# Kernel optimization log

Measured on AMD Instinct MI355X. Metric: run time of the kernel, lower is better.

The kernel has to match this reference:

```python
import jax, jax.numpy as jnp
import numpy as np

N, E, D = 100000, 200000, 300
NUM_EDGE_EMB = [6, 3]
BN_EPS = 1e-5


def setup_inputs() -> dict:
    key = jax.random.key(0)
    ks = jax.random.split(key, 10)
    return {
        "node_feats": jax.random.normal(ks[0], (N, D), jnp.float32),
        "src": jax.random.randint(ks[1], (E,), 0, N),
        "dst": jax.random.randint(ks[2], (E,), 0, N),
        "edge_feat0": jax.random.randint(ks[3], (E,), 0, NUM_EDGE_EMB[0]),
        "edge_feat1": jax.random.randint(ks[4], (E,), 0, NUM_EDGE_EMB[1]),
        # edge 'MLP' with num_layers=1 == Linear(num_emb, D) on one-hot indices
        "emb_w0": jax.random.normal(ks[5], (NUM_EDGE_EMB[0], D), jnp.float32) * 0.1,
        "emb_b0": jnp.zeros((D,), jnp.float32),
        "emb_w1": jax.random.normal(ks[6], (NUM_EDGE_EMB[1], D), jnp.float32) * 0.1,
        "emb_b1": jnp.zeros((D,), jnp.float32),
        # GIN update MLP: Linear(D, 2D) -> ReLU -> Linear(2D, D)
        "mlp_w1": jax.random.normal(ks[7], (D, 2 * D), jnp.float32) * (1.0 / np.sqrt(D)),
        "mlp_b1": jnp.zeros((2 * D,), jnp.float32),
        "mlp_w2": jax.random.normal(ks[8], (2 * D, D), jnp.float32) * (1.0 / np.sqrt(2 * D)),
        "mlp_b2": jnp.zeros((D,), jnp.float32),
        "bn_gamma": jnp.ones((D,), jnp.float32),
        "bn_beta": jnp.zeros((D,), jnp.float32),
    }


def reference(node_feats, src, dst, edge_feat0, edge_feat1,
              emb_w0, emb_b0, emb_w1, emb_b1,
              mlp_w1, mlp_b1, mlp_w2, mlp_b2,
              bn_gamma, bn_beta):
    n = node_feats.shape[0]
    # sum of per-variable edge embeddings (one-hot linear == lookup + bias)
    edge_emb = (emb_w0[edge_feat0] + emb_b0) + (emb_w1[edge_feat1] + emb_b1)  # (E, D)
    # u_add_e message, sum-reduce onto destination nodes
    msgs = node_feats[src] + edge_emb                                         # (E, D)
    agg = jax.ops.segment_sum(msgs, dst, num_segments=n)                      # (N, D)
    # GIN update MLP
    h = jax.nn.relu(agg @ mlp_w1 + mlp_b1)
    h = h @ mlp_w2 + mlp_b2
    # BatchNorm1d (training-mode forward: biased batch stats)
    mean = jnp.mean(h, axis=0)
    var = jnp.var(h, axis=0)
    h = (h - mean) * jax.lax.rsqrt(var + BN_EPS) * bn_gamma + bn_beta
    return h
```

## Files before the change

### kernel.cpp

```cpp
#include <hip/hip_runtime.h>
#include <stdint.h>


typedef __attribute__((ext_vector_type(8))) short short8;
typedef __attribute__((ext_vector_type(4))) short short4v;
typedef __attribute__((ext_vector_type(4))) float float4v;

__device__ inline float b2f(unsigned short u) {
  union { unsigned int i; float f; } v; v.i = ((unsigned int)u) << 16; return v.f;
}
__device__ inline unsigned short f2b(float f) {
  union { float f; unsigned int i; } v; v.f = f;
  unsigned int i = v.i;
  i += 0x7fffu + ((i >> 16) & 1u);
  return (unsigned short)(i >> 16);
}

__device__ __forceinline__ void gl_lds16(const short* g, short* l) {
  __builtin_amdgcn_global_load_lds(
      (const __attribute__((address_space(1))) unsigned int*)g,
      (__attribute__((address_space(3))) unsigned int*)l,
      16, 0, 0);
}

__global__ void transpose_pad(const float* __restrict__ in, short* __restrict__ out,
                              int R, int C, int outStride, int total) {
  int idx = blockIdx.x * blockDim.x + threadIdx.x;
  if (idx >= total) return;
  int r = idx / C, c = idx - r * C;
  out[(size_t)c * outStride + r] = (short)f2b(in[idx]);
}

__global__ void nf2b(const float* __restrict__ nf, unsigned short* __restrict__ nfb,
                     int D, int ldab, int total) {
  int idx = blockIdx.x * blockDim.x + threadIdx.x;
  if (idx >= total) return;
  const int chunks = ldab >> 3;
  int node = idx / chunks, c = idx - node * chunks;
  int d = c * 8;
  short4v r0 = {0, 0, 0, 0}, r1 = {0, 0, 0, 0};
  const float* p = &nf[(size_t)node * D + d];
  if (d + 3 < D) {
    float4v v = *(const float4v*)p;
    r0[0] = (short)f2b(v[0]); r0[1] = (short)f2b(v[1]);
    r0[2] = (short)f2b(v[2]); r0[3] = (short)f2b(v[3]);
  }
  if (d + 7 < D) {
    float4v v = *(const float4v*)(p + 4);
    r1[0] = (short)f2b(v[0]); r1[1] = (short)f2b(v[1]);
    r1[2] = (short)f2b(v[2]); r1[3] = (short)f2b(v[3]);
  }
  unsigned short* op = &nfb[(size_t)node * ldab + d];
  *(short4v*)op = r0;
  *(short4v*)(op + 4) = r1;
}

__global__ void build_w01b(const float* __restrict__ w0, const float* __restrict__ w1,
                           const float* __restrict__ b0, const float* __restrict__ b1,
                           unsigned short* __restrict__ w01b, float* __restrict__ bb01,
                           int D, int NUM1, int ldab, int total) {
  int i = blockIdx.x * blockDim.x + threadIdx.x;
  if (i >= total) return;
  int f01 = i / ldab, d = i - f01 * ldab;
  int f0 = f01 / NUM1, f1 = f01 - f0 * NUM1;
  float v = (d < D) ? (w0[f0 * D + d] + w1[f1 * D + d]) : 0.f;
  w01b[i] = f2b(v);
  if (f01 == 0) bb01[d] = (d < D) ? (b0[d] + b1[d]) : 0.f;
}

__global__ void count_deg(const int* __restrict__ dst, int* __restrict__ deg, int E) {
  int e = blockIdx.x * blockDim.x + threadIdx.x;
  if (e < E) atomicAdd(&deg[dst[e]], 1);
}

__global__ void scan1(const int* __restrict__ deg, int* __restrict__ offp,
                      int* __restrict__ bsum, int n) {
  __shared__ int sh[256];
  const int t = threadIdx.x;
  const int base = blockIdx.x * 1024 + t * 4;
  int v[4], s = 0;
#pragma unroll
  for (int j = 0; j < 4; ++j) { int i = base + j; v[j] = (i < n) ? deg[i] : 0; s += v[j]; }
  sh[t] = s;
  __syncthreads();
  for (int d = 1; d < 256; d <<= 1) {
    int x = (t >= d) ? sh[t - d] : 0;
    __syncthreads();
    sh[t] += x;
    __syncthreads();
  }
  int excl = (t > 0) ? sh[t - 1] : 0;
  if (t == 255) bsum[blockIdx.x] = sh[255];
#pragma unroll
  for (int j = 0; j < 4; ++j) { int i = base + j; if (i < n) offp[i] = excl; excl += v[j]; }
}

__global__ void scan2(int* __restrict__ bsum, int nb) {
  __shared__ int sh[256];
  const int t = threadIdx.x;
  sh[t] = (t < nb) ? bsum[t] : 0;
  __syncthreads();
  for (int d = 1; d < 256; d <<= 1) {
    int x = (t >= d) ? sh[t - d] : 0;
    __syncthreads();
    sh[t] += x;
    __syncthreads();
  }
  if (t < nb) bsum[t] = (t > 0) ? sh[t - 1] : 0;
}

__global__ void fill_csr(const int* __restrict__ dst, const int* __restrict__ src,
                         const int* __restrict__ ef0, const int* __restrict__ ef1,
                         const int* __restrict__ offp, const int* __restrict__ bsum,
                         int* __restrict__ tmp, int2* __restrict__ ebp, int NUM1, int E) {
  int e = blockIdx.x * blockDim.x + threadIdx.x;
  if (e >= E) return;
  int dn = dst[e];
  int pos = offp[dn] + bsum[dn >> 10] + atomicAdd(&tmp[dn], 1);
  ebp[pos] = make_int2(src[e], ef0[e] * NUM1 + ef1[e]);
}

__global__ void gather_agg(const unsigned short* __restrict__ nfb,
                           const unsigned short* __restrict__ w01b,
                           const float* __restrict__ bb01,
                           const int* __restrict__ deg, const int* __restrict__ offp,
                           const int* __restrict__ bsum, const int2* __restrict__ ebp,
                           unsigned short* __restrict__ aggb,
                           int ldab, int total) {
  int idx = blockIdx.x * blockDim.x + threadIdx.x;
  if (idx >= total) return;
  const int segs = ldab >> 5;
  int node = idx / segs;
  int c = idx - node * segs;
  int d = c * 32;
  int dg = deg[node];
  int o = offp[node] + bsum[node >> 10];
  float acc[32];
#pragma unroll
  for (int k = 0; k < 32; ++k) acc[k] = 0.f;
  for (int j = 0; j < dg; ++j) {
    int2 p = ebp[o + j];
    const unsigned short* np = &nfb[(size_t)p.x * ldab + d];
    const unsigned short* wp = &w01b[(size_t)p.y * ldab + d];
#pragma unroll
    for (int q = 0; q < 4; ++q) {
      short8 nv = *(const short8*)(np + q * 8);
      short8 wv = *(const short8*)(wp + q * 8);
#pragma unroll
      for (int k = 0; k < 8; ++k)
        acc[q * 8 + k] += b2f((unsigned short)nv[k]) + b2f((unsigned short)wv[k]);
    }
  }
  float fdg = (float)dg;
#pragma unroll
  for (int q = 0; q < 8; ++q) {
    float4v bb = *(const float4v*)&bb01[d + q * 4];
#pragma unroll
    for (int k = 0; k < 4; ++k) acc[q * 4 + k] += fdg * bb[k];
  }
#pragma unroll
  for (int q = 0; q < 4; ++q) {
    short8 r;
#pragma unroll
    for (int k = 0; k < 8; ++k) r[k] = (short)f2b(acc[q * 8 + k]);
    *(short8*)&aggb[(size_t)node * ldab + d + q * 8] = r;
  }
}

template<bool RELU, bool STATS, bool CF32>
__global__ __launch_bounds__(256, 6)
void gemm_lds(const short* __restrict__ A, int lda,
              const short* __restrict__ BT, int ldbt,
              const float* __restrict__ bias,
              void* __restrict__ Cv, int ldc, int storeN,
              int M, int Nn, int KP, int ncolb,
              float* __restrict__ colsum, float* __restrict__ colsumsq) {
  constexpr int BM = 128, BN = 64, BK = 32;
  __shared__ __align__(16) short Al[2][BM * BK];
  __shared__ __align__(16) short Bl[2][BN * BK];

  const int nwg = gridDim.x;
  const int b = blockIdx.x;
  const int qq = nwg >> 3, rr = nwg & 7;
  const int xcd = b & 7, ii = b >> 3;
  const int w = ((xcd < rr) ? xcd * (qq + 1) : rr * (qq + 1) + (xcd - rr) * qq) + ii;
  const int by = w / ncolb, bx = w - by * ncolb;
  const int m0 = by * BM, n0 = bx * BN;

  const int t = threadIdx.x;
  const int wave = t >> 6, lane = t & 63, quad = lane >> 4, lr = lane & 15;
  const int wm = (wave >> 1) * 64, wn = (wave & 1) * 32;

  const int au = lane & 3;
  const int arow0 = (wave * 2 + 0) * 16 + (lane >> 2);
  const int arow1 = (wave * 2 + 1) * 16 + (lane >> 2);
  const int asw0 = au ^ ((arow0 ^ (arow0 >> 2)) & 3);
  const int asw1 = au ^ ((arow1 ^ (arow1 >> 2)) & 3);
  const short* asrc0 = A + (size_t)(m0 + arow0) * lda + asw0 * 8;
  const short* asrc1 = A + (size_t)(m0 + arow1) * lda + asw1 * 8;
  const int adst0 = (wave * 2 + 0) * 512;
  const int adst1 = (wave * 2 + 1) * 512;
  const int brow = wave * 16 + (lane >> 2);
  const int bsw = au ^ ((brow ^ (brow >> 2)) & 3);
  const short* bsrc = BT + (size_t)(n0 + brow) * ldbt + bsw * 8;
  const int bdst = wave * 512;

  int aoff[4], boff[2];
#pragma unroll
  for (int mi = 0; mi < 4; ++mi) {
    int r = wm + mi * 16 + lr;
    aoff[mi] = r * BK + (quad ^ ((r ^ (r >> 2)) & 3)) * 8;
  }
#pragma unroll
  for (int ni = 0; ni < 2; ++ni) {
    int r = wn + ni * 16 + lr;
    boff[ni] = r * BK + (quad ^ ((r ^ (r >> 2)) & 3)) * 8;
  }

  const float4v fzero = {0.f, 0.f, 0.f, 0.f};
  float4v acc[4][2];
#pragma unroll
  for (int mi = 0; mi < 4; ++mi) {
    acc[mi][0] = fzero; acc[mi][1] = fzero;
  }

  const int KPfull = KP & ~63;
  for (int k0 = 0; k0 < KPfull; k0 += 2 * BK) {
    __syncthreads();
    gl_lds16(asrc0 + k0, (short*)&Al[0][adst0]);
    gl_lds16(asrc1 + k0, (short*)&Al[0][adst1]);
    gl_lds16(bsrc + k0, (short*)&Bl[0][bdst]);
    gl_lds16(asrc0 + k0 + BK, (short*)&Al[1][adst0]);
    gl_lds16(asrc1 + k0 + BK, (short*)&Al[1][adst1]);
    gl_lds16(bsrc + k0 + BK, (short*)&Bl[1][bdst]);
    __syncthreads();
#pragma unroll
    for (int p = 0; p < 2; ++p) {
      short8 af[4], bfr[2];
#pragma unroll
      for (int mi = 0; mi < 4; ++mi) af[mi] = *(const short8*)&Al[p][aoff[mi]];
#pragma unroll
      for (int ni = 0; ni < 2; ++ni) bfr[ni] = *(const short8*)&Bl[p][boff[ni]];
#pragma unroll
      for (int mi = 0; mi < 4; ++mi) {
        acc[mi][0] = __builtin_amdgcn_mfma_f32_16x16x32_bf16(af[mi], bfr[0], acc[mi][0], 0, 0, 0);
        acc[mi][1] = __builtin_amdgcn_mfma_f32_16x16x32_bf16(af[mi], bfr[1], acc[mi][1], 0, 0, 0);
      }
    }
  }
  if (KP & 63) {
    int k0 = KPfull;
    __syncthreads();
    gl_lds16(asrc0 + k0, (short*)&Al[0][adst0]);
    gl_lds16(asrc1 + k0, (short*)&Al[0][adst1]);
    gl_lds16(bsrc + k0, (short*)&Bl[0][bdst]);
    __syncthreads();
    short8 af[4], bfr[2];
#pragma unroll
    for (int mi = 0; mi < 4; ++mi) af[mi] = *(const short8*)&Al[0][aoff[mi]];
#pragma unroll
    for (int ni = 0; ni < 2; ++ni) bfr[ni] = *(const short8*)&Bl[0][boff[ni]];
#pragma unroll
    for (int mi = 0; mi < 4; ++mi) {
      acc[mi][0] = __builtin_amdgcn_mfma_f32_16x16x32_bf16(af[mi], bfr[0], acc[mi][0], 0, 0, 0);
      acc[mi][1] = __builtin_amdgcn_mfma_f32_16x16x32_bf16(af[mi], bfr[1], acc[mi][1], 0, 0, 0);
    }
  }

#pragma unroll
  for (int ni = 0; ni < 2; ++ni) {
    int gn = n0 + wn + ni * 16 + lr;
    bool store_c = (gn < storeN);
    bool ncol = (gn < Nn);
    float bv = ncol ? bias[gn] : 0.f;
    float s = 0.f, q = 0.f;
#pragma unroll
    for (int mi = 0; mi < 4; ++mi) {
      int gmb = m0 + wm + mi * 16 + quad * 4;
#pragma unroll
      for (int r = 0; r < 4; ++r) {
        int gm = gmb + r;
        float v = acc[mi][ni][r] + bv;
        if (RELU) v = fmaxf(v, 0.f);
        if (gm < M && store_c) {
          if constexpr (CF32) ((float*)Cv)[(size_t)gm * ldc + gn] = v;
          else ((unsigned short*)Cv)[(size_t)gm * ldc + gn] = f2b(v);
          if (STATS && ncol) { s += v; q += v * v; }
        }
      }
    }
    if constexpr (STATS) {
      s += __shfl_xor(s, 16); q += __shfl_xor(q, 16);
      s += __shfl_xor(s, 32); q += __shfl_xor(q, 32);
      if (quad == 0 && ncol) {
        unsafeAtomicAdd(&colsum[gn], s);
        unsafeAtomicAdd(&colsumsq[gn], q);
      }
    }
  }
}

__global__ void bn_finalize(const float* __restrict__ colsum, const float* __restrict__ colsumsq,
                            const float* __restrict__ gamma, const float* __restrict__ beta,
                            float2* __restrict__ ss, int D, float invN) {
  int d = blockIdx.x * blockDim.x + threadIdx.x;
  if (d >= D) return;
  float mean = colsum[d] * invN;
  float var = fmaxf(colsumsq[d] * invN - mean * mean, 0.f);
  float sc = rsqrtf(var + 1e-5f) * gamma[d];
  float sh = beta[d] - mean * sc;
  ss[d] = make_float2(sc, sh);
}

__global__ void bn_apply4(float4v* __restrict__ out, const float2* __restrict__ ss,
                          int total4, int cquads) {
  int idx = blockIdx.x * blockDim.x + threadIdx.x;
  if (idx >= total4) return;
  int c = (idx % cquads) * 4;
  float4v v = out[idx];
  float2 p0 = ss[c], p1 = ss[c + 1], p2 = ss[c + 2], p3 = ss[c + 3];
  v[0] = v[0] * p0.x + p0.y;
  v[1] = v[1] * p1.x + p1.y;
  v[2] = v[2] * p2.x + p2.y;
  v[3] = v[3] * p3.x + p3.y;
  out[idx] = v;
}

__global__ void bn_apply1(float* __restrict__ out, const float2* __restrict__ ss,
                          int total, int D) {
  int idx = blockIdx.x * blockDim.x + threadIdx.x;
  if (idx >= total) return;
  float2 p = ss[idx % D];
  out[idx] = out[idx] * p.x + p.y;
}

extern "C" void kernel_launch(void* const* d_in, const int* in_sizes, int n_in,
                              void* d_out, int out_size, void* d_ws, size_t ws_size,
                              hipStream_t stream) {
  const float* nf  = (const float*)d_in[0];
  const int*   src = (const int*)d_in[1];
  const int*   dst = (const int*)d_in[2];
  const int*   ef0 = (const int*)d_in[3];
  const int*   ef1 = (const int*)d_in[4];
  const float* ew0 = (const float*)d_in[5];
  const float* eb0 = (const float*)d_in[6];
  const float* ew1 = (const float*)d_in[7];
  const float* eb1 = (const float*)d_in[8];
  const float* w1  = (const float*)d_in[9];
  const float* b1  = (const float*)d_in[10];
  const float* w2  = (const float*)d_in[11];
  const float* b2  = (const float*)d_in[12];
  const float* gam = (const float*)d_in[13];
  const float* bet = (const float*)d_in[14];

  const int D = in_sizes[13];
  const int N = in_sizes[0] / D;
  const int E = in_sizes[1];
  const int H = in_sizes[10];
  const int NUM0 = in_sizes[5] / D;
  const int NUM1 = in_sizes[7] / D;
  const int KP1 = (D + 63) / 64 * 64;
  const int KP2 = (H + 31) / 32 * 32;
  const int NCB1 = (H + 63) / 64;
  const int NCB2 = (D + 63) / 64;
  const int BROWS1 = NCB1 * 64;
  const int BROWS2 = NCB2 * 64;
  const int nrowb = (N + 127) / 128;
  const int MP = nrowb * 128;
  const int nb  = (N + 1023) / 1024;

  char* ws = (char*)d_ws;
  size_t off = 0;
  float* colsum   = (float*)(ws + off); off += 4096;
  float* colsumsq = (float*)(ws + off); off += 4096;
  short* wT1      = (short*)(ws + off); off += (size_t)BROWS1 * KP1 * 2;
  short* wT2      = (short*)(ws + off); off += (size_t)BROWS2 * KP2 * 2;
  int*   deg      = (int*)(ws + off);   off += (size_t)N * 4;
  int*   tmp      = (int*)(ws + off);   off += (size_t)N * 4;
  size_t zero_bytes = off;
  float2* ss      = (float2*)(ws + off); off += 4096;
  unsigned short* w01b = (unsigned short*)(ws + off); off += (size_t)NUM0 * NUM1 * KP1 * 2;
  float* bb01     = (float*)(ws + off);  off += (size_t)KP1 * 4;
  int*   offp     = (int*)(ws + off);    off += (size_t)N * 4;
  int*   bsum     = (int*)(ws + off);    off += 4096;
  int2*  ebp      = (int2*)(ws + off);   off += (size_t)E * 8;
  unsigned short* aggb = (unsigned short*)(ws + off); off += (size_t)MP * KP1 * 2;
  short* h1       = (short*)(ws + off);  off += (size_t)MP * KP2 * 2;
  unsigned short* nfb = (unsigned short*)h1;

  hipMemsetAsync(d_ws, 0, zero_bytes, stream);

  {
    int tot = D * H;
    transpose_pad<<<(tot + 255) / 256, 256, 0, stream>>>(w1, wT1, D, H, KP1, tot);
  }
  {
    int tot = H * D;
    transpose_pad<<<(tot + 255) / 256, 256, 0, stream>>>(w2, wT2, H, D, KP2, tot);
  }
  {
    int tot = NUM0 * NUM1 * KP1;
    build_w01b<<<(tot + 255) / 256, 256, 0, stream>>>(ew0, ew1, eb0, eb1,
                                                      w01b, bb01, D, NUM1, KP1, tot);
  }
  {
    int tot = N * (KP1 / 8);
    nf2b<<<(tot + 255) / 256, 256, 0, stream>>>(nf, nfb, D, KP1, tot);
  }
  count_deg<<<(E + 255) / 256, 256, 0, stream>>>(dst, deg, E);
  scan1<<<nb, 256, 0, stream>>>(deg, offp, bsum, N);
  scan2<<<1, 256, 0, stream>>>(bsum, nb);
  fill_csr<<<(E + 255) / 256, 256, 0, stream>>>(dst, src, ef0, ef1, offp, bsum, tmp,
                                                ebp, NUM1, E);
  {
    int total = N * (KP1 / 32);
    gather_agg<<<(total + 255) / 256, 256, 0, stream>>>(
        nfb, w01b, bb01, deg, offp, bsum, ebp, aggb, KP1, total);
  }
  {
    gemm_lds<true, false, false><<<nrowb * NCB1, 256, 0, stream>>>(
        (const short*)aggb, KP1, wT1, KP1, b1,
        h1, KP2, KP2, N, H, KP1, NCB1, nullptr, nullptr);
  }
  {
    gemm_lds<false, true, true><<<nrowb * NCB2, 256, 0, stream>>>(
        h1, KP2, wT2, KP2, b2,
        d_out, D, D, N, D, KP2, NCB2, colsum, colsumsq);
  }
  bn_finalize<<<(D + 255) / 256, 256, 0, stream>>>(colsum, colsumsq, gam, bet, ss, D,
                                                   1.0f / (float)N);
  if ((D & 3) == 0) {
    int total4 = N * (D / 4);
    bn_apply4<<<(total4 + 255) / 256, 256, 0, stream>>>((float4v*)d_out, ss, total4, D / 4);
  } else {
    int tot = N * D;
    bn_apply1<<<(tot + 255) / 256, 256, 0, stream>>>((float*)d_out, ss, tot, D);
  }
}
```

Before: 559.8 us.

## Replace direct global-to-LDS loads with register-staged loads into padded LDS

The bf16 MFMA GEMM now copies A and B tiles through registers into a padded shared-memory layout (row stride 40), instead of using async global_load_lds with XOR swizzling. It uses a single buffer and one 32-wide K step per iteration, which doubles the number of barriers per K. The occupancy hint in the launch bounds is dropped, and K padding for the first GEMM is rounded to 32 instead of 64. The aim is simpler, conflict-free LDS access. The cost is extra register traffic and barriers, and less overlap between loads and MFMA work.

```diff
diff --git a/kernel.cpp b/kernel.cpp
--- a/kernel.cpp
+++ b/kernel.cpp
@@ -14,13 +14,6 @@
   unsigned int i = v.i;
   i += 0x7fffu + ((i >> 16) & 1u);
   return (unsigned short)(i >> 16);
-}
-
-__device__ __forceinline__ void gl_lds16(const short* g, short* l) {
-  __builtin_amdgcn_global_load_lds(
-      (const __attribute__((address_space(1))) unsigned int*)g,
-      (__attribute__((address_space(3))) unsigned int*)l,
-      16, 0, 0);
 }
 
 __global__ void transpose_pad(const float* __restrict__ in, short* __restrict__ out,
@@ -168,16 +161,16 @@
 }
 
 template<bool RELU, bool STATS, bool CF32>
-__global__ __launch_bounds__(256, 6)
-void gemm_lds(const short* __restrict__ A, int lda,
-              const short* __restrict__ BT, int ldbt,
-              const float* __restrict__ bias,
-              void* __restrict__ Cv, int ldc, int storeN,
-              int M, int Nn, int KP, int ncolb,
-              float* __restrict__ colsum, float* __restrict__ colsumsq) {
-  constexpr int BM = 128, BN = 64, BK = 32;
-  __shared__ __align__(16) short Al[2][BM * BK];
-  __shared__ __align__(16) short Bl[2][BN * BK];
+__global__ __launch_bounds__(256)
+void gemm_rs(const short* __restrict__ A, int lda,
+             const short* __restrict__ BT, int ldbt,
+             const float* __restrict__ bias,
+             void* __restrict__ Cv, int ldc, int storeN,
+             int M, int Nn, int KP, int ncolb,
+             float* __restrict__ colsum, float* __restrict__ colsumsq) {
+  constexpr int BM = 128, BN = 64, BK = 32, SA = 40;
+  __shared__ __align__(16) short Al[BM * SA];
+  __shared__ __align__(16) short Bl[BN * SA];
 
   const int nwg = gridDim.x;
   const int b = blockIdx.x;
@@ -191,32 +184,6 @@
   const int wave = t >> 6, lane = t & 63, quad = lane >> 4, lr = lane & 15;
   const int wm = (wave >> 1) * 64, wn = (wave & 1) * 32;
 
-  const int au = lane & 3;
-  const int arow0 = (wave * 2 + 0) * 16 + (lane >> 2);
-  const int arow1 = (wave * 2 + 1) * 16 + (lane >> 2);
-  const int asw0 = au ^ ((arow0 ^ (arow0 >> 2)) & 3);
-  const int asw1 = au ^ ((arow1 ^ (arow1 >> 2)) & 3);
-  const short* asrc0 = A + (size_t)(m0 + arow0) * lda + asw0 * 8;
-  const short* asrc1 = A + (size_t)(m0 + arow1) * lda + asw1 * 8;
-  const int adst0 = (wave * 2 + 0) * 512;
-  const int adst1 = (wave * 2 + 1) * 512;
-  const int brow = wave * 16 + (lane >> 2);
-  const int bsw = au ^ ((brow ^ (brow >> 2)) & 3);
-  const short* bsrc = BT + (size_t)(n0 + brow) * ldbt + bsw * 8;
-  const int bdst = wave * 512;
-
-  int aoff[4], boff[2];
-#pragma unroll
-  for (int mi = 0; mi < 4; ++mi) {
-    int r = wm + mi * 16 + lr;
-    aoff[mi] = r * BK + (quad ^ ((r ^ (r >> 2)) & 3)) * 8;
-  }
-#pragma unroll
-  for (int ni = 0; ni < 2; ++ni) {
-    int r = wn + ni * 16 + lr;
-    boff[ni] = r * BK + (quad ^ ((r ^ (r >> 2)) & 3)) * 8;
-  }
-
   const float4v fzero = {0.f, 0.f, 0.f, 0.f};
   float4v acc[4][2];
 #pragma unroll
@@ -224,42 +191,28 @@
     acc[mi][0] = fzero; acc[mi][1] = fzero;
   }
 
-  const int KPfull = KP & ~63;
-  for (int k0 = 0; k0 < KPfull; k0 += 2 * BK) {
-    __syncthreads();
-    gl_lds16(asrc0 + k0, (short*)&Al[0][adst0]);
-    gl_lds16(asrc1 + k0, (short*)&Al[0][adst1]);
-    gl_lds16(bsrc + k0, (short*)&Bl[0][bdst]);
-    gl_lds16(asrc0 + k0 + BK, (short*)&Al[1][adst0]);
-    gl_lds16(asrc1 + k0 + BK, (short*)&Al[1][adst1]);
-    gl_lds16(bsrc + k0 + BK, (short*)&Bl[1][bdst]);
-    __syncthreads();
-#pragma unroll
-    for (int p = 0; p < 2; ++p) {
-      short8 af[4], bfr[2];
-#pragma unroll
-      for (int mi = 0; mi < 4; ++mi) af[mi] = *(const short8*)&Al[p][aoff[mi]];
-#pragma unroll
-      for (int ni = 0; ni < 2; ++ni) bfr[ni] = *(const short8*)&Bl[p][boff[ni]];
-#pragma unroll
-      for (int mi = 0; mi < 4; ++mi) {
-        acc[mi][0] = __builtin_amdgcn_mfma_f32_16x16x32_bf16(af[mi], bfr[0], acc[mi][0], 0, 0, 0);
-        acc[mi][1] = __builtin_amdgcn_mfma_f32_16x16x32_bf16(af[mi], bfr[1], acc[mi][1], 0, 0, 0);
-      }
-    }
-  }
-  if (KP & 63) {
-    int k0 = KPfull;
-    __syncthreads();
-    gl_lds16(asrc0 + k0, (short*)&Al[0][adst0]);
-    gl_lds16(asrc1 + k0, (short*)&Al[0][adst1]);
-    gl_lds16(bsrc + k0, (short*)&Bl[0][bdst]);
+  const int sr0 = t >> 2, sc0 = (t & 3) << 3;
+  const int sr1 = (t + 256) >> 2;
+  const short* asrc0 = A + (size_t)(m0 + sr0) * lda + sc0;
+  const short* asrc1 = A + (size_t)(m0 + sr1) * lda + sc0;
+  const short* bsrc = BT + (size_t)(n0 + sr0) * ldbt + sc0;
+  short* adst0 = &Al[sr0 * SA + sc0];
+  short* adst1 = &Al[sr1 * SA + sc0];
+  short* bdst = &Bl[sr0 * SA + sc0];
+
+  for (int k0 = 0; k0 < KP; k0 += BK) {
+    __syncthreads();
+    *(short8*)adst0 = *(const short8*)(asrc0 + k0);
+    *(short8*)adst1 = *(const short8*)(asrc1 + k0);
+    *(short8*)bdst = *(const short8*)(bsrc + k0);
     __syncthreads();
     short8 af[4], bfr[2];
 #pragma unroll
-    for (int mi = 0; mi < 4; ++mi) af[mi] = *(const short8*)&Al[0][aoff[mi]];
-#pragma unroll
-    for (int ni = 0; ni < 2; ++ni) bfr[ni] = *(const short8*)&Bl[0][boff[ni]];
+    for (int mi = 0; mi < 4; ++mi)
+      af[mi] = *(short8*)&Al[(wm + mi * 16 + lr) * SA + quad * 8];
+#pragma unroll
+    for (int ni = 0; ni < 2; ++ni)
+      bfr[ni] = *(short8*)&Bl[(wn + ni * 16 + lr) * SA + quad * 8];
 #pragma unroll
     for (int mi = 0; mi < 4; ++mi) {
       acc[mi][0] = __builtin_amdgcn_mfma_f32_16x16x32_bf16(af[mi], bfr[0], acc[mi][0], 0, 0, 0);
@@ -359,7 +312,7 @@
   const int H = in_sizes[10];
   const int NUM0 = in_sizes[5] / D;
   const int NUM1 = in_sizes[7] / D;
-  const int KP1 = (D + 63) / 64 * 64;
+  const int KP1 = (D + 31) / 32 * 32;
   const int KP2 = (H + 31) / 32 * 32;
   const int NCB1 = (H + 63) / 64;
   const int NCB2 = (D + 63) / 64;
@@ -418,12 +371,12 @@
         nfb, w01b, bb01, deg, offp, bsum, ebp, aggb, KP1, total);
   }
   {
-    gemm_lds<true, false, false><<<nrowb * NCB1, 256, 0, stream>>>(
+    gemm_rs<true, false, false><<<nrowb * NCB1, 256, 0, stream>>>(
         (const short*)aggb, KP1, wT1, KP1, b1,
         h1, KP2, KP2, N, H, KP1, NCB1, nullptr, nullptr);
   }
   {
-    gemm_lds<false, true, true><<<nrowb * NCB2, 256, 0, stream>>>(
+    gemm_rs<false, true, true><<<nrowb * NCB2, 256, 0, stream>>>(
         h1, KP2, wT2, KP2, b2,
         d_out, D, D, N, D, KP2, NCB2, colsum, colsumsq);
   }
```

New measurement: 571.2 us. +2.0%, slower.
